# Kernel optimization log

Hardware: AMD Instinct MI355X
Metric: run time of the kernel (lower is better)

The kernel has to match this reference:

```python
import jax, jax.numpy as jnp
import numpy as np

N_INST = 64  # number of distinct instance colors generated (color = 4*label, label 0 = background)
LAMBDA_SEP = 300.0


def setup_inputs() -> dict:
    key = jax.random.key(0)
    k1, k2 = jax.random.split(key)
    B, H, W = 4, 768, 768
    labels = jax.random.randint(k1, (B, H, W), 0, N_INST)
    labels = labels.at[:, :8, :8].set(0)  # guarantee background pixels exist (torch code assumes bg_pred is set)
    # target colors: (4*l, 4*l, 4*l) in [0, 252]; background label 0 -> (0,0,0)
    target = jnp.broadcast_to((labels * 4).astype(jnp.float32)[:, None, :, :], (B, 3, H, W))
    prediction = jax.random.uniform(k2, (B, 3, H, W), dtype=jnp.float32) * 255.0
    no_bg = jnp.zeros((B,), dtype=bool)
    return {"prediction": prediction, "target": target, "no_bg": no_bg}


def _huber(x, c):
    # elementwise huber, delta=1.0 (torch default)
    d = jnp.abs(x - c)
    return jnp.where(d < 1.0, 0.5 * d * d, d - 0.5)


def _per_image(P, L, nobg):
    # P: [N,3] predicted colors, L: [N] int instance labels (0 = background)
    N = P.shape[0]
    counts = jax.ops.segment_sum(jnp.ones((N,), P.dtype), L, num_segments=N_INST)  # [K]
    safe = jnp.maximum(counts, 1.0)
    means = jax.ops.segment_sum(P, L, num_segments=N_INST) / safe[:, None]  # [K,3]
    # intra-instance huber toward constant target (255 for instances, 0 for background), mean over 3*count elems
    h255 = _huber(P, 255.0).sum(-1)  # [N]
    h0 = _huber(P, 0.0).sum(-1)
    var = jax.ops.segment_sum(h255, L, num_segments=N_INST) / (3.0 * safe)
    var0 = jax.ops.segment_sum(h0, L, num_segments=N_INST) / (3.0 * safe)
    var = var.at[0].set(var0[0])
    # pixel -> instance-mean squared distances [N,K] (separation term)
    D = jnp.sum((P[:, None, :] - means[None, :, :]) ** 2, axis=-1)
    inv = LAMBDA_SEP / (1.0 + D)  # [N,K]
    bg_mask = (L == 0).astype(P.dtype)  # [N]
    bg_cnt = bg_mask.sum()
    nbg_cnt = jnp.asarray(N, P.dtype) - bg_cnt
    # non-bg instance k: mean over background pixels of 300/(1+||p - mean_k||^2)
    sep = (bg_mask @ inv) / jnp.maximum(bg_cnt, 1.0)  # [K]
    # background instance: mean over non-background pixels vs bg mean
    sep0 = ((1.0 - bg_mask) @ inv[:, 0]) / jnp.maximum(nbg_cnt, 1.0)
    sep = sep.at[0].set(sep0)
    w = 10.0 / jnp.sqrt(safe)
    present = counts > 0
    included = present.at[0].set(jnp.logical_and(present[0], jnp.logical_not(nobg)))
    incl = included.astype(P.dtype)
    ct = jnp.maximum(incl.sum(), 1.0)
    return jnp.sum(incl * (var + w * sep)) / ct


def reference(prediction, target, no_bg):
    B = prediction.shape[0]
    # recover integer instance labels from color map (generation: color = 4*label on all 3 channels)
    labels = jnp.round(target[:, 0] / 4.0).astype(jnp.int32).reshape(B, -1)  # [B,N]
    P = jnp.transpose(prediction, (0, 2, 3, 1)).reshape(B, -1, 3)  # [B,N,3]
    losses = jax.vmap(_per_image)(P, labels, no_bg)
    return jnp.mean(losses)
```

## Files before the change

### kernel.cpp

```cpp
#include <hip/hip_runtime.h>

#define NINST 64
#define ACC_STRIDE 512
#define OFF_CNT  0
#define OFF_SUM  64
#define OFF_H255 256
#define OFF_H0   320
#define LAMBDA_SEP 300.0f

#define P1_GX 192
#define P1_THREADS 512
#define P1_WAVES (P1_THREADS / 64)
#define P2_GX 128
#define P3_GX 32
#define P3_TILE 256
#define CNT_STRIDE 64
#define BGBUF 512

__device__ __forceinline__ float huber1(float x, float c) {
    float d = fabsf(x - c);
    return d < 1.0f ? 0.5f * d * d : d - 0.5f;
}

__global__ __launch_bounds__(P1_THREADS)
void k_pass1(const float* __restrict__ pred, const float* __restrict__ targ,
             float* __restrict__ acc, unsigned* __restrict__ bgcnt,
             float* __restrict__ bglist, int maxbg, int N) {
    __shared__ float4 s_stage[P1_WAVES][256];
    __shared__ float4 s_red[P1_WAVES][NINST];
    __shared__ float s_corr255[NINST];
    __shared__ float s_corr0;
    __shared__ float s_bgbuf[BGBUF * 3];
    __shared__ unsigned s_bgn;
    __shared__ unsigned s_base;
    int tid = threadIdx.x;
    int lane = tid & 63;
    int wv = tid >> 6;
    if (tid < NINST) s_corr255[tid] = 0.0f;
    if (tid == 0) { s_corr0 = 0.0f; s_bgn = 0u; }
    __syncthreads();

    int b = blockIdx.y;
    const float* bp = pred + (size_t)b * 3 * N;
    const float* bt = targ + (size_t)b * 3 * N;
    const float4* t0 = (const float4*)bt;
    const float4* p0 = (const float4*)bp;
    const float4* p1 = (const float4*)(bp + N);
    const float4* p2 = (const float4*)(bp + 2 * N);
    unsigned* bgc = &bgcnt[(size_t)b * CNT_STRIDE];
    float* bgl = bglist + (size_t)b * maxbg * 3;
    float* g = acc + (size_t)b * ACC_STRIDE;

    float cnt = 0.0f, sx = 0.0f, sy = 0.0f, sz = 0.0f;
    int M = N >> 2;
    int stride = gridDim.x * blockDim.x;
    for (int base = blockIdx.x * blockDim.x + wv * 64; base < M; base += stride) {
        int i = base + lane;
        float xx[4], yy[4], zz[4];
        int labs[4];
        if (i < M) {
            float4 t = t0[i], a = p0[i], c = p1[i], d = p2[i];
            float tt[4] = {t.x, t.y, t.z, t.w};
            xx[0] = a.x; xx[1] = a.y; xx[2] = a.z; xx[3] = a.w;
            yy[0] = c.x; yy[1] = c.y; yy[2] = c.z; yy[3] = c.w;
            zz[0] = d.x; zz[1] = d.y; zz[2] = d.z; zz[3] = d.w;
#pragma unroll
            for (int j = 0; j < 4; j++) {
                int lab = (int)(tt[j] * 0.25f + 0.5f);
                labs[j] = lab;
                float dx = 255.0f - xx[j], dy = 255.0f - yy[j], dz = 255.0f - zz[j];
                float corr = 0.0f;
                if (dx < 1.0f) { float e = 1.0f - dx; corr += 0.5f * e * e; }
                if (dy < 1.0f) { float e = 1.0f - dy; corr += 0.5f * e * e; }
                if (dz < 1.0f) { float e = 1.0f - dz; corr += 0.5f * e * e; }
                if (corr != 0.0f) atomicAdd(&s_corr255[lab], corr);
                if (lab == 0) {
                    float c0 = 0.0f;
                    if (xx[j] < 1.0f) { float e = 1.0f - xx[j]; c0 += 0.5f * e * e; }
                    if (yy[j] < 1.0f) { float e = 1.0f - yy[j]; c0 += 0.5f * e * e; }
                    if (zz[j] < 1.0f) { float e = 1.0f - zz[j]; c0 += 0.5f * e * e; }
                    if (c0 != 0.0f) atomicAdd(&s_corr0, c0);
                    unsigned idx = atomicAdd(&s_bgn, 1u);
                    if (idx < BGBUF) {
                        s_bgbuf[idx * 3 + 0] = xx[j];
                        s_bgbuf[idx * 3 + 1] = yy[j];
                        s_bgbuf[idx * 3 + 2] = zz[j];
                    } else {
                        unsigned gi = atomicAdd(bgc, 1u);
                        if ((int)gi < maxbg) {
                            bgl[(size_t)gi * 3 + 0] = xx[j];
                            bgl[(size_t)gi * 3 + 1] = yy[j];
                            bgl[(size_t)gi * 3 + 2] = zz[j];
                        }
                    }
                }
            }
        } else {
#pragma unroll
            for (int j = 0; j < 4; j++) { xx[j] = yy[j] = zz[j] = 0.0f; labs[j] = -1; }
        }
#pragma unroll
        for (int j = 0; j < 4; j++)
            s_stage[wv][j * 64 + lane] =
                make_float4(xx[j], yy[j], zz[j], __int_as_float(labs[j]));
#pragma unroll 8
        for (int s = 0; s < 256; s++) {
            float4 v = s_stage[wv][s];
            float m = (__float_as_int(v.w) == lane) ? 1.0f : 0.0f;
            cnt += m;
            sx = fmaf(m, v.x, sx);
            sy = fmaf(m, v.y, sy);
            sz = fmaf(m, v.z, sz);
        }
    }

    s_red[wv][lane] = make_float4(cnt, sx, sy, sz);
    __syncthreads();

    unsigned nloc = s_bgn < (unsigned)BGBUF ? s_bgn : (unsigned)BGBUF;
    if (tid == 0) s_base = atomicAdd(bgc, nloc);
    __syncthreads();
    {
        unsigned base3 = s_base * 3u;
        unsigned lim3 = (unsigned)maxbg * 3u;
        for (unsigned i = tid; i < nloc * 3u; i += blockDim.x) {
            if (base3 + i < lim3) bgl[base3 + i] = s_bgbuf[i];
        }
    }

    if (tid < NINST) {
        float c = 0.0f, x = 0.0f, y = 0.0f, z = 0.0f;
#pragma unroll
        for (int w = 0; w < P1_WAVES; w++) {
            float4 r = s_red[w][tid];
            c += r.x; x += r.y; y += r.z; z += r.w;
        }
        float s3 = x + y + z;
        atomicAdd(&g[OFF_CNT + tid], c);
        atomicAdd(&g[OFF_SUM + tid * 3 + 0], x);
        atomicAdd(&g[OFF_SUM + tid * 3 + 1], y);
        atomicAdd(&g[OFF_SUM + tid * 3 + 2], z);
        atomicAdd(&g[OFF_H255 + tid], 763.5f * c - s3 + s_corr255[tid]);
        if (tid == 0) atomicAdd(&g[OFF_H0], s3 - 1.5f * c + s_corr0);
    }

    if (blockIdx.x == 0 && tid < (N & 3)) {
        int i = (M << 2) + tid;
        float t = bt[i], x = bp[i], y = bp[N + i], z = bp[2 * N + i];
        int lab = (int)(t * 0.25f + 0.5f);
        atomicAdd(&g[OFF_CNT + lab], 1.0f);
        atomicAdd(&g[OFF_SUM + lab * 3 + 0], x);
        atomicAdd(&g[OFF_SUM + lab * 3 + 1], y);
        atomicAdd(&g[OFF_SUM + lab * 3 + 2], z);
        atomicAdd(&g[OFF_H255 + lab], huber1(x, 255.f) + huber1(y, 255.f) + huber1(z, 255.f));
        if (lab == 0) {
            atomicAdd(&g[OFF_H0], huber1(x, 0.f) + huber1(y, 0.f) + huber1(z, 0.f));
            unsigned gi = atomicAdd(bgc, 1u);
            if ((int)gi < maxbg) {
                bgl[(size_t)gi * 3 + 0] = x;
                bgl[(size_t)gi * 3 + 1] = y;
                bgl[(size_t)gi * 3 + 2] = z;
            }
        }
    }
}

__global__ void k_pass2(const float* __restrict__ pred, const float* __restrict__ targ,
                        const float* __restrict__ acc, float* __restrict__ p2part, int N) {
    __shared__ float s_w[16];
    int tid = threadIdx.x;
    int b = blockIdx.y;
    const float* g = acc + (size_t)b * ACC_STRIDE;
    float safe0 = fmaxf(g[OFF_CNT + 0], 1.0f);
    float m0x = g[OFF_SUM + 0] / safe0;
    float m0y = g[OFF_SUM + 1] / safe0;
    float m0z = g[OFF_SUM + 2] / safe0;

    const float* base_p = pred + (size_t)b * 3 * N;
    const float* base_t = targ + (size_t)b * 3 * N;
    const float4* p0 = (const float4*)(base_p);
    const float4* p1 = (const float4*)(base_p + N);
    const float4* p2 = (const float4*)(base_p + 2 * N);
    const float4* t0 = (const float4*)(base_t);

    float local = 0.0f;
    int M = N >> 2;
    for (int i = blockIdx.x * blockDim.x + tid; i < M; i += gridDim.x * blockDim.x) {
        float4 t = t0[i], a = p0[i], c = p1[i], d = p2[i];
        float ts[4] = {t.x, t.y, t.z, t.w};
        float xs[4] = {a.x, a.y, a.z, a.w};
        float ys[4] = {c.x, c.y, c.z, c.w};
        float zs[4] = {d.x, d.y, d.z, d.w};
#pragma unroll
        for (int j = 0; j < 4; j++) {
            float dx = xs[j] - m0x, dy = ys[j] - m0y, dz = zs[j] - m0z;
            float D = dx * dx + dy * dy + dz * dz;
            float m = (ts[j] > 2.0f) ? LAMBDA_SEP : 0.0f;
            local = fmaf(m, __builtin_amdgcn_rcpf(1.0f + D), local);
        }
    }
    if (blockIdx.x == 0) {
        for (int i = (M << 2) + tid; i < N; i += blockDim.x) {
            float dx = base_p[i] - m0x, dy = base_p[N + i] - m0y, dz = base_p[2 * N + i] - m0z;
            float D = dx * dx + dy * dy + dz * dz;
            float m = (base_t[i] > 2.0f) ? LAMBDA_SEP : 0.0f;
            local = fmaf(m, __builtin_amdgcn_rcpf(1.0f + D), local);
        }
    }
#pragma unroll
    for (int o = 32; o > 0; o >>= 1) local += __shfl_down(local, o, 64);
    int wv = tid >> 6;
    if ((tid & 63) == 0) s_w[wv] = local;
    __syncthreads();
    if (tid == 0) {
        float s = 0.0f;
        int nw = blockDim.x >> 6;
        for (int i = 0; i < nw; i++) s += s_w[i];
        p2part[(size_t)b * P2_GX + blockIdx.x] = s;
    }
}

__global__ void k_pass3(const float* __restrict__ bglist, const unsigned* __restrict__ bgcnt,
                        const float* __restrict__ acc, float* __restrict__ p3part, int maxbg) {
    __shared__ float s_px[P3_TILE * 3];
    __shared__ float s_part[4][NINST];
    int tid = threadIdx.x;
    int lane = tid & 63;
    int wv = tid >> 6;
    int b = blockIdx.y;
    const float* g = acc + (size_t)b * ACC_STRIDE;
    float safe = fmaxf(g[OFF_CNT + lane], 1.0f);
    float mx = g[OFF_SUM + lane * 3 + 0] / safe;
    float my = g[OFF_SUM + lane * 3 + 1] / safe;
    float mz = g[OFF_SUM + lane * 3 + 2] / safe;

    int nb = min((int)bgcnt[(size_t)b * CNT_STRIDE], maxbg);
    const float* bgl = bglist + (size_t)b * maxbg * 3;

    float lacc = 0.0f;
    int ntiles = (nb + P3_TILE - 1) / P3_TILE;
    for (int tile = blockIdx.x; tile < ntiles; tile += gridDim.x) {
        int base = tile * P3_TILE;
        int cnt = min(P3_TILE, nb - base);
        __syncthreads();
        for (int i = tid; i < cnt * 3; i += blockDim.x) s_px[i] = bgl[(size_t)base * 3 + i];
        __syncthreads();
        int lim = cnt - wv * 64;
        lim = lim < 0 ? 0 : (lim > 64 ? 64 : lim);
        const float* px = &s_px[wv * 64 * 3];
        for (int j = 0; j < lim; j++) {
            float x = px[j * 3 + 0];
            float y = px[j * 3 + 1];
            float z = px[j * 3 + 2];
            float dx = x - mx, dy = y - my, dz = z - mz;
            float D = dx * dx + dy * dy + dz * dz;
            lacc += LAMBDA_SEP * __builtin_amdgcn_rcpf(1.0f + D);
        }
    }
    s_part[wv][lane] = lacc;
    __syncthreads();
    if (tid < NINST) {
        p3part[((size_t)b * P3_GX + blockIdx.x) * NINST + tid] =
            s_part[0][tid] + s_part[1][tid] + s_part[2][tid] + s_part[3][tid];
    }
}

__global__ void k_final(const float* __restrict__ acc, const float* __restrict__ p2part,
                        const float* __restrict__ p3part, const unsigned char* __restrict__ nobg,
                        float* __restrict__ out, int N, int B) {
    int tid = threadIdx.x;
    float total = 0.0f;
    for (int b = 0; b < B; b++) {
        const float* g = acc + (size_t)b * ACC_STRIDE;
        float c = g[OFF_CNT + tid];
        float c0 = g[OFF_CNT + 0];
        bool incl = (c > 0.0f);
        if (tid == 0 && nobg[b] != 0) incl = false;
        float safe = fmaxf(c, 1.0f);
        float var = (tid == 0 ? g[OFF_H0] : g[OFF_H255 + tid]) / (3.0f * safe);
        float sepnum;
        if (tid == 0) {
            float s = 0.0f;
            for (int i = 0; i < P2_GX; i++) s += p2part[(size_t)b * P2_GX + i];
            sepnum = s;
        } else {
            float s = 0.0f;
#pragma unroll
            for (int j = 0; j < P3_GX; j++) s += p3part[((size_t)b * P3_GX + j) * NINST + tid];
            sepnum = s;
        }
        float denom = (tid == 0) ? fmaxf((float)N - c0, 1.0f) : fmaxf(c0, 1.0f);
        float sep = sepnum / denom;
        float w = 10.0f / sqrtf(safe);
        float term = incl ? (var + w * sep) : 0.0f;
        float cnt = incl ? 1.0f : 0.0f;
#pragma unroll
        for (int o = 32; o > 0; o >>= 1) {
            term += __shfl_down(term, o, 64);
            cnt += __shfl_down(cnt, o, 64);
        }
        if (tid == 0) total += term / fmaxf(cnt, 1.0f);
    }
    if (tid == 0) out[0] = total / (float)B;
}

extern "C" void kernel_launch(void* const* d_in, const int* in_sizes, int n_in,
                              void* d_out, int out_size, void* d_ws, size_t ws_size,
                              hipStream_t stream) {
    const float* pred = (const float*)d_in[0];
    const float* targ = (const float*)d_in[1];
    const unsigned char* nobg = (const unsigned char*)d_in[2];
    float* out = (float*)d_out;

    int B = in_sizes[2];
    int N = in_sizes[0] / (3 * B);

    float* acc = (float*)d_ws;
    size_t acc_bytes = (size_t)B * ACC_STRIDE * sizeof(float);
    unsigned* bgcnt = (unsigned*)((char*)d_ws + acc_bytes);
    size_t head = acc_bytes + 4096;
    float* p2part = (float*)((char*)d_ws + head);
    size_t p2_bytes = (size_t)B * P2_GX * sizeof(float);
    float* p3part = p2part + (size_t)B * P2_GX;
    size_t p3_bytes = (size_t)B * P3_GX * NINST * sizeof(float);
    size_t list_off = head + p2_bytes + p3_bytes;
    list_off = (list_off + 255) & ~(size_t)255;
    float* bglist = (float*)((char*)d_ws + list_off);

    int maxbg = 0;
    if (ws_size > list_off) {
        size_t cap = (ws_size - list_off) / ((size_t)B * 3 * sizeof(float));
        maxbg = (int)(cap < (size_t)131072 ? cap : (size_t)131072);
    }

    hipMemsetAsync(d_ws, 0, head, stream);

    dim3 g1(P1_GX, B);
    k_pass1<<<g1, dim3(P1_THREADS), 0, stream>>>(pred, targ, acc, bgcnt, bglist, maxbg, N);
    dim3 g2(P2_GX, B);
    k_pass2<<<g2, dim3(1024), 0, stream>>>(pred, targ, acc, p2part, N);
    dim3 g3(P3_GX, B);
    k_pass3<<<g3, dim3(256), 0, stream>>>(bglist, bgcnt, acc, p3part, maxbg);
    k_final<<<dim3(1), dim3(64), 0, stream>>>(acc, p2part, p3part, nobg, out, N, B);
}
```

Baseline: 77.83 us.

## Split per-wave segment sum across lane groups with 8-label register accumulators

```diff
diff --git a/kernel.cpp b/kernel.cpp
--- a/kernel.cpp
+++ b/kernel.cpp
@@ -8,7 +8,7 @@
 #define OFF_H0   320
 #define LAMBDA_SEP 300.0f
 
-#define P1_GX 192
+#define P1_GX 128
 #define P1_THREADS 512
 #define P1_WAVES (P1_THREADS / 64)
 #define P2_GX 128
@@ -22,7 +22,7 @@
     return d < 1.0f ? 0.5f * d * d : d - 0.5f;
 }
 
-__global__ __launch_bounds__(P1_THREADS)
+__global__ __launch_bounds__(P1_THREADS, 4)
 void k_pass1(const float* __restrict__ pred, const float* __restrict__ targ,
              float* __restrict__ acc, unsigned* __restrict__ bgcnt,
              float* __restrict__ bglist, int maxbg, int N) {
@@ -36,6 +36,8 @@
     int tid = threadIdx.x;
     int lane = tid & 63;
     int wv = tid >> 6;
+    int grp = lane >> 3;
+    int s8 = (lane & 7) << 3;
     if (tid < NINST) s_corr255[tid] = 0.0f;
     if (tid == 0) { s_corr0 = 0.0f; s_bgn = 0u; }
     __syncthreads();
@@ -51,7 +53,10 @@
     float* bgl = bglist + (size_t)b * maxbg * 3;
     float* g = acc + (size_t)b * ACC_STRIDE;
 
-    float cnt = 0.0f, sx = 0.0f, sy = 0.0f, sz = 0.0f;
+    float cnt[8], sx[8], sy[8], sz[8];
+#pragma unroll
+    for (int t = 0; t < 8; t++) { cnt[t] = 0.0f; sx[t] = 0.0f; sy[t] = 0.0f; sz[t] = 0.0f; }
+
     int M = N >> 2;
     int stride = gridDim.x * blockDim.x;
     for (int base = blockIdx.x * blockDim.x + wv * 64; base < M; base += stride) {
@@ -103,18 +108,50 @@
         for (int j = 0; j < 4; j++)
             s_stage[wv][j * 64 + lane] =
                 make_float4(xx[j], yy[j], zz[j], __int_as_float(labs[j]));
-#pragma unroll 8
-        for (int s = 0; s < 256; s++) {
-            float4 v = s_stage[wv][s];
-            float m = (__float_as_int(v.w) == lane) ? 1.0f : 0.0f;
-            cnt += m;
-            sx = fmaf(m, v.x, sx);
-            sy = fmaf(m, v.y, sy);
-            sz = fmaf(m, v.z, sz);
-        }
-    }
-
-    s_red[wv][lane] = make_float4(cnt, sx, sy, sz);
+#pragma unroll 4
+        for (int j = 0; j < 32; j++) {
+            float4 v = s_stage[wv][(j << 3) + grp];
+            int rel = __float_as_int(v.w) - s8;
+#pragma unroll
+            for (int t = 0; t < 8; t++) {
+                float m = (rel == t) ? 1.0f : 0.0f;
+                cnt[t] += m;
+                sx[t] = fmaf(m, v.x, sx[t]);
+                sy[t] = fmaf(m, v.y, sy[t]);
+                sz[t] = fmaf(m, v.z, sz[t]);
+            }
+        }
+    }
+
+#pragma unroll
+    for (int q = 0; q < 4; q++)
+        s_stage[wv][(lane << 2) + q] = make_float4(cnt[q], sx[q], sy[q], sz[q]);
+    __syncthreads();
+    {
+        int l = lane & 31;
+        float4 ra = make_float4(0.0f, 0.0f, 0.0f, 0.0f);
+#pragma unroll
+        for (int gg = 0; gg < 8; gg++) {
+            float4 p = s_stage[wv][gg * 32 + l];
+            ra.x += p.x; ra.y += p.y; ra.z += p.z; ra.w += p.w;
+        }
+        if (lane < 32) s_red[wv][((l >> 2) << 3) + (l & 3)] = ra;
+    }
+    __syncthreads();
+#pragma unroll
+    for (int q = 0; q < 4; q++)
+        s_stage[wv][(lane << 2) + q] = make_float4(cnt[q + 4], sx[q + 4], sy[q + 4], sz[q + 4]);
+    __syncthreads();
+    {
+        int l = lane & 31;
+        float4 rb = make_float4(0.0f, 0.0f, 0.0f, 0.0f);
+#pragma unroll
+        for (int gg = 0; gg < 8; gg++) {
+            float4 p = s_stage[wv][gg * 32 + l];
+            rb.x += p.x; rb.y += p.y; rb.z += p.z; rb.w += p.w;
+        }
+        if (lane >= 32) s_red[wv][((l >> 2) << 3) + 4 + (l & 3)] = rb;
+    }
     __syncthreads();
 
     unsigned nloc = s_bgn < (unsigned)BGBUF ? s_bgn : (unsigned)BGBUF;
```

Result: no change. 78.55 us (+0.9%).

## Use per-wave LDS atomic histograms in pass1 and fuse pass2/pass3 kernels

Applied to the files above, without the earlier changes.

```diff
diff --git a/kernel.cpp b/kernel.cpp
--- a/kernel.cpp
+++ b/kernel.cpp
@@ -8,34 +8,35 @@
 #define OFF_H0   320
 #define LAMBDA_SEP 300.0f
 
-#define P1_GX 192
+#define P1_GX 256
 #define P1_THREADS 512
 #define P1_WAVES (P1_THREADS / 64)
+#define HSTRIDE 5
 #define P2_GX 128
-#define P3_GX 32
-#define P3_TILE 256
+#define P23_THREADS 1024
+#define P3B 8
+#define P3_TILE 1024
 #define CNT_STRIDE 64
-#define BGBUF 512
+#define BGBUF 256
 
 __device__ __forceinline__ float huber1(float x, float c) {
     float d = fabsf(x - c);
     return d < 1.0f ? 0.5f * d * d : d - 0.5f;
 }
 
-__global__ __launch_bounds__(P1_THREADS)
+__global__ __launch_bounds__(P1_THREADS, 8)
 void k_pass1(const float* __restrict__ pred, const float* __restrict__ targ,
              float* __restrict__ acc, unsigned* __restrict__ bgcnt,
              float* __restrict__ bglist, int maxbg, int N) {
-    __shared__ float4 s_stage[P1_WAVES][256];
-    __shared__ float4 s_red[P1_WAVES][NINST];
+    __shared__ float s_hist[P1_WAVES * NINST * HSTRIDE];
     __shared__ float s_corr255[NINST];
     __shared__ float s_corr0;
     __shared__ float s_bgbuf[BGBUF * 3];
     __shared__ unsigned s_bgn;
     __shared__ unsigned s_base;
     int tid = threadIdx.x;
-    int lane = tid & 63;
     int wv = tid >> 6;
+    for (int i = tid; i < P1_WAVES * NINST * HSTRIDE; i += P1_THREADS) s_hist[i] = 0.0f;
     if (tid < NINST) s_corr255[tid] = 0.0f;
     if (tid == 0) { s_corr0 = 0.0f; s_bgn = 0u; }
     __syncthreads();
@@ -50,71 +51,55 @@
     unsigned* bgc = &bgcnt[(size_t)b * CNT_STRIDE];
     float* bgl = bglist + (size_t)b * maxbg * 3;
     float* g = acc + (size_t)b * ACC_STRIDE;
-
-    float cnt = 0.0f, sx = 0.0f, sy = 0.0f, sz = 0.0f;
+    float* myhist = &s_hist[wv * NINST * HSTRIDE];
+
     int M = N >> 2;
     int stride = gridDim.x * blockDim.x;
-    for (int base = blockIdx.x * blockDim.x + wv * 64; base < M; base += stride) {
-        int i = base + lane;
-        float xx[4], yy[4], zz[4];
-        int labs[4];
-        if (i < M) {
-            float4 t = t0[i], a = p0[i], c = p1[i], d = p2[i];
-            float tt[4] = {t.x, t.y, t.z, t.w};
-            xx[0] = a.x; xx[1] = a.y; xx[2] = a.z; xx[3] = a.w;
-            yy[0] = c.x; yy[1] = c.y; yy[2] = c.z; yy[3] = c.w;
-            zz[0] = d.x; zz[1] = d.y; zz[2] = d.z; zz[3] = d.w;
-#pragma unroll
-            for (int j = 0; j < 4; j++) {
-                int lab = (int)(tt[j] * 0.25f + 0.5f);
-                labs[j] = lab;
-                float dx = 255.0f - xx[j], dy = 255.0f - yy[j], dz = 255.0f - zz[j];
+    for (int i = blockIdx.x * blockDim.x + tid; i < M; i += stride) {
+        float4 t = t0[i], a = p0[i], c = p1[i], d = p2[i];
+        float tt[4] = {t.x, t.y, t.z, t.w};
+        float xx[4] = {a.x, a.y, a.z, a.w};
+        float yy[4] = {c.x, c.y, c.z, c.w};
+        float zz[4] = {d.x, d.y, d.z, d.w};
+#pragma unroll
+        for (int j = 0; j < 4; j++) {
+            int lab = (int)(tt[j] * 0.25f + 0.5f);
+            float* hb = &myhist[lab * HSTRIDE];
+            atomicAdd(hb + 0, xx[j]);
+            atomicAdd(hb + 1, yy[j]);
+            atomicAdd(hb + 2, zz[j]);
+            atomicAdd(hb + 3, 1.0f);
+            float m3 = fmaxf(fmaxf(xx[j], yy[j]), zz[j]);
+            if (m3 > 254.0f) {
                 float corr = 0.0f;
-                if (dx < 1.0f) { float e = 1.0f - dx; corr += 0.5f * e * e; }
-                if (dy < 1.0f) { float e = 1.0f - dy; corr += 0.5f * e * e; }
-                if (dz < 1.0f) { float e = 1.0f - dz; corr += 0.5f * e * e; }
-                if (corr != 0.0f) atomicAdd(&s_corr255[lab], corr);
-                if (lab == 0) {
-                    float c0 = 0.0f;
-                    if (xx[j] < 1.0f) { float e = 1.0f - xx[j]; c0 += 0.5f * e * e; }
-                    if (yy[j] < 1.0f) { float e = 1.0f - yy[j]; c0 += 0.5f * e * e; }
-                    if (zz[j] < 1.0f) { float e = 1.0f - zz[j]; c0 += 0.5f * e * e; }
-                    if (c0 != 0.0f) atomicAdd(&s_corr0, c0);
-                    unsigned idx = atomicAdd(&s_bgn, 1u);
-                    if (idx < BGBUF) {
-                        s_bgbuf[idx * 3 + 0] = xx[j];
-                        s_bgbuf[idx * 3 + 1] = yy[j];
-                        s_bgbuf[idx * 3 + 2] = zz[j];
-                    } else {
-                        unsigned gi = atomicAdd(bgc, 1u);
-                        if ((int)gi < maxbg) {
-                            bgl[(size_t)gi * 3 + 0] = xx[j];
-                            bgl[(size_t)gi * 3 + 1] = yy[j];
-                            bgl[(size_t)gi * 3 + 2] = zz[j];
-                        }
+                float ex = xx[j] - 254.0f, ey = yy[j] - 254.0f, ez = zz[j] - 254.0f;
+                if (ex > 0.0f) corr += 0.5f * ex * ex;
+                if (ey > 0.0f) corr += 0.5f * ey * ey;
+                if (ez > 0.0f) corr += 0.5f * ez * ez;
+                atomicAdd(&s_corr255[lab], corr);
+            }
+            if (lab == 0) {
+                float c0 = 0.0f;
+                if (xx[j] < 1.0f) { float e = 1.0f - xx[j]; c0 += 0.5f * e * e; }
+                if (yy[j] < 1.0f) { float e = 1.0f - yy[j]; c0 += 0.5f * e * e; }
+                if (zz[j] < 1.0f) { float e = 1.0f - zz[j]; c0 += 0.5f * e * e; }
+                if (c0 != 0.0f) atomicAdd(&s_corr0, c0);
+                unsigned idx = atomicAdd(&s_bgn, 1u);
+                if (idx < BGBUF) {
+                    s_bgbuf[idx * 3 + 0] = xx[j];
+                    s_bgbuf[idx * 3 + 1] = yy[j];
+                    s_bgbuf[idx * 3 + 2] = zz[j];
+                } else {
+                    unsigned gi = atomicAdd(bgc, 1u);
+                    if ((int)gi < maxbg) {
+                        bgl[(size_t)gi * 3 + 0] = xx[j];
+                        bgl[(size_t)gi * 3 + 1] = yy[j];
+                        bgl[(size_t)gi * 3 + 2] = zz[j];
                     }
                 }
             }
-        } else {
-#pragma unroll
-            for (int j = 0; j < 4; j++) { xx[j] = yy[j] = zz[j] = 0.0f; labs[j] = -1; }
-        }
-#pragma unroll
-        for (int j = 0; j < 4; j++)
-            s_stage[wv][j * 64 + lane] =
-                make_float4(xx[j], yy[j], zz[j], __int_as_float(labs[j]));
-#pragma unroll 8
-        for (int s = 0; s < 256; s++) {
-            float4 v = s_stage[wv][s];
-            float m = (__float_as_int(v.w) == lane) ? 1.0f : 0.0f;
-            cnt += m;
-            sx = fmaf(m, v.x, sx);
-            sy = fmaf(m, v.y, sy);
-            sz = fmaf(m, v.z, sz);
-        }
-    }
-
-    s_red[wv][lane] = make_float4(cnt, sx, sy, sz);
+        }
+    }
     __syncthreads();
 
     unsigned nloc = s_bgn < (unsigned)BGBUF ? s_bgn : (unsigned)BGBUF;
@@ -132,8 +117,8 @@
         float c = 0.0f, x = 0.0f, y = 0.0f, z = 0.0f;
 #pragma unroll
         for (int w = 0; w < P1_WAVES; w++) {
-            float4 r = s_red[w][tid];
-            c += r.x; x += r.y; y += r.z; z += r.w;
+            const float* hb = &s_hist[(w * NINST + tid) * HSTRIDE];
+            x += hb[0]; y += hb[1]; z += hb[2]; c += hb[3];
         }
         float s3 = x + y + z;
         atomicAdd(&g[OFF_CNT + tid], c);
@@ -165,103 +150,104 @@
     }
 }
 
-__global__ void k_pass2(const float* __restrict__ pred, const float* __restrict__ targ,
-                        const float* __restrict__ acc, float* __restrict__ p2part, int N) {
+__global__ void k_pass23(const float* __restrict__ pred, const float* __restrict__ targ,
+                         const float* __restrict__ acc, const float* __restrict__ bglist,
+                         const unsigned* __restrict__ bgcnt, float* __restrict__ p2part,
+                         float* __restrict__ p3part, int maxbg, int N) {
     __shared__ float s_w[16];
+    __shared__ float s_px[P3_TILE * 3];
+    __shared__ float s_part[16][NINST];
     int tid = threadIdx.x;
     int b = blockIdx.y;
     const float* g = acc + (size_t)b * ACC_STRIDE;
-    float safe0 = fmaxf(g[OFF_CNT + 0], 1.0f);
-    float m0x = g[OFF_SUM + 0] / safe0;
-    float m0y = g[OFF_SUM + 1] / safe0;
-    float m0z = g[OFF_SUM + 2] / safe0;
-
-    const float* base_p = pred + (size_t)b * 3 * N;
-    const float* base_t = targ + (size_t)b * 3 * N;
-    const float4* p0 = (const float4*)(base_p);
-    const float4* p1 = (const float4*)(base_p + N);
-    const float4* p2 = (const float4*)(base_p + 2 * N);
-    const float4* t0 = (const float4*)(base_t);
-
-    float local = 0.0f;
-    int M = N >> 2;
-    for (int i = blockIdx.x * blockDim.x + tid; i < M; i += gridDim.x * blockDim.x) {
-        float4 t = t0[i], a = p0[i], c = p1[i], d = p2[i];
-        float ts[4] = {t.x, t.y, t.z, t.w};
-        float xs[4] = {a.x, a.y, a.z, a.w};
-        float ys[4] = {c.x, c.y, c.z, c.w};
-        float zs[4] = {d.x, d.y, d.z, d.w};
-#pragma unroll
-        for (int j = 0; j < 4; j++) {
-            float dx = xs[j] - m0x, dy = ys[j] - m0y, dz = zs[j] - m0z;
-            float D = dx * dx + dy * dy + dz * dz;
-            float m = (ts[j] > 2.0f) ? LAMBDA_SEP : 0.0f;
-            local = fmaf(m, __builtin_amdgcn_rcpf(1.0f + D), local);
-        }
-    }
-    if (blockIdx.x == 0) {
-        for (int i = (M << 2) + tid; i < N; i += blockDim.x) {
-            float dx = base_p[i] - m0x, dy = base_p[N + i] - m0y, dz = base_p[2 * N + i] - m0z;
-            float D = dx * dx + dy * dy + dz * dz;
-            float m = (base_t[i] > 2.0f) ? LAMBDA_SEP : 0.0f;
-            local = fmaf(m, __builtin_amdgcn_rcpf(1.0f + D), local);
-        }
-    }
-#pragma unroll
-    for (int o = 32; o > 0; o >>= 1) local += __shfl_down(local, o, 64);
-    int wv = tid >> 6;
-    if ((tid & 63) == 0) s_w[wv] = local;
-    __syncthreads();
-    if (tid == 0) {
-        float s = 0.0f;
-        int nw = blockDim.x >> 6;
-        for (int i = 0; i < nw; i++) s += s_w[i];
-        p2part[(size_t)b * P2_GX + blockIdx.x] = s;
-    }
-}
-
-__global__ void k_pass3(const float* __restrict__ bglist, const unsigned* __restrict__ bgcnt,
-                        const float* __restrict__ acc, float* __restrict__ p3part, int maxbg) {
-    __shared__ float s_px[P3_TILE * 3];
-    __shared__ float s_part[4][NINST];
-    int tid = threadIdx.x;
-    int lane = tid & 63;
-    int wv = tid >> 6;
-    int b = blockIdx.y;
-    const float* g = acc + (size_t)b * ACC_STRIDE;
-    float safe = fmaxf(g[OFF_CNT + lane], 1.0f);
-    float mx = g[OFF_SUM + lane * 3 + 0] / safe;
-    float my = g[OFF_SUM + lane * 3 + 1] / safe;
-    float mz = g[OFF_SUM + lane * 3 + 2] / safe;
-
-    int nb = min((int)bgcnt[(size_t)b * CNT_STRIDE], maxbg);
-    const float* bgl = bglist + (size_t)b * maxbg * 3;
-
-    float lacc = 0.0f;
-    int ntiles = (nb + P3_TILE - 1) / P3_TILE;
-    for (int tile = blockIdx.x; tile < ntiles; tile += gridDim.x) {
-        int base = tile * P3_TILE;
-        int cnt = min(P3_TILE, nb - base);
+
+    if (blockIdx.x < P2_GX) {
+        float safe0 = fmaxf(g[OFF_CNT + 0], 1.0f);
+        float m0x = g[OFF_SUM + 0] / safe0;
+        float m0y = g[OFF_SUM + 1] / safe0;
+        float m0z = g[OFF_SUM + 2] / safe0;
+
+        const float* base_p = pred + (size_t)b * 3 * N;
+        const float* base_t = targ + (size_t)b * 3 * N;
+        const float4* p0 = (const float4*)(base_p);
+        const float4* p1 = (const float4*)(base_p + N);
+        const float4* p2 = (const float4*)(base_p + 2 * N);
+        const float4* t0 = (const float4*)(base_t);
+
+        float local = 0.0f;
+        int M = N >> 2;
+        for (int i = blockIdx.x * blockDim.x + tid; i < M; i += P2_GX * blockDim.x) {
+            float4 t = t0[i], a = p0[i], c = p1[i], d = p2[i];
+            float ts[4] = {t.x, t.y, t.z, t.w};
+            float xs[4] = {a.x, a.y, a.z, a.w};
+            float ys[4] = {c.x, c.y, c.z, c.w};
+            float zs[4] = {d.x, d.y, d.z, d.w};
+#pragma unroll
+            for (int j = 0; j < 4; j++) {
+                float dx = xs[j] - m0x, dy = ys[j] - m0y, dz = zs[j] - m0z;
+                float D = dx * dx + dy * dy + dz * dz;
+                float m = (ts[j] > 2.0f) ? LAMBDA_SEP : 0.0f;
+                local = fmaf(m, __builtin_amdgcn_rcpf(1.0f + D), local);
+            }
+        }
+        if (blockIdx.x == 0) {
+            for (int i = (M << 2) + tid; i < N; i += blockDim.x) {
+                float dx = base_p[i] - m0x, dy = base_p[N + i] - m0y, dz = base_p[2 * N + i] - m0z;
+                float D = dx * dx + dy * dy + dz * dz;
+                float m = (base_t[i] > 2.0f) ? LAMBDA_SEP : 0.0f;
+                local = fmaf(m, __builtin_amdgcn_rcpf(1.0f + D), local);
+            }
+        }
+#pragma unroll
+        for (int o = 32; o > 0; o >>= 1) local += __shfl_down(local, o, 64);
+        int wv = tid >> 6;
+        if ((tid & 63) == 0) s_w[wv] = local;
         __syncthreads();
-        for (int i = tid; i < cnt * 3; i += blockDim.x) s_px[i] = bgl[(size_t)base * 3 + i];
+        if (tid == 0) {
+            float s = 0.0f;
+            for (int i = 0; i < (P23_THREADS >> 6); i++) s += s_w[i];
+            p2part[(size_t)b * P2_GX + blockIdx.x] = s;
+        }
+    } else {
+        int bx = blockIdx.x - P2_GX;
+        int lane = tid & 63;
+        int wv = tid >> 6;
+        float safe = fmaxf(g[OFF_CNT + lane], 1.0f);
+        float mx = g[OFF_SUM + lane * 3 + 0] / safe;
+        float my = g[OFF_SUM + lane * 3 + 1] / safe;
+        float mz = g[OFF_SUM + lane * 3 + 2] / safe;
+
+        int nb = min((int)bgcnt[(size_t)b * CNT_STRIDE], maxbg);
+        const float* bgl = bglist + (size_t)b * maxbg * 3;
+
+        float lacc = 0.0f;
+        int ntiles = (nb + P3_TILE - 1) / P3_TILE;
+        for (int tile = bx; tile < ntiles; tile += P3B) {
+            int base = tile * P3_TILE;
+            int cnt = min(P3_TILE, nb - base);
+            __syncthreads();
+            for (int i = tid; i < cnt * 3; i += blockDim.x) s_px[i] = bgl[(size_t)base * 3 + i];
+            __syncthreads();
+            int lim = cnt - wv * 64;
+            lim = lim < 0 ? 0 : (lim > 64 ? 64 : lim);
+            const float* px = &s_px[wv * 64 * 3];
+            for (int j = 0; j < lim; j++) {
+                float x = px[j * 3 + 0];
+                float y = px[j * 3 + 1];
+                float z = px[j * 3 + 2];
+                float dx = x - mx, dy = y - my, dz = z - mz;
+                float D = dx * dx + dy * dy + dz * dz;
+                lacc += LAMBDA_SEP * __builtin_amdgcn_rcpf(1.0f + D);
+            }
+        }
+        s_part[wv][lane] = lacc;
         __syncthreads();
-        int lim = cnt - wv * 64;
-        lim = lim < 0 ? 0 : (lim > 64 ? 64 : lim);
-        const float* px = &s_px[wv * 64 * 3];
-        for (int j = 0; j < lim; j++) {
-            float x = px[j * 3 + 0];
-            float y = px[j * 3 + 1];
-            float z = px[j * 3 + 2];
-            float dx = x - mx, dy = y - my, dz = z - mz;
-            float D = dx * dx + dy * dy + dz * dz;
-            lacc += LAMBDA_SEP * __builtin_amdgcn_rcpf(1.0f + D);
-        }
-    }
-    s_part[wv][lane] = lacc;
-    __syncthreads();
-    if (tid < NINST) {
-        p3part[((size_t)b * P3_GX + blockIdx.x) * NINST + tid] =
-            s_part[0][tid] + s_part[1][tid] + s_part[2][tid] + s_part[3][tid];
+        if (tid < NINST) {
+            float s = 0.0f;
+#pragma unroll
+            for (int w = 0; w < 16; w++) s += s_part[w][tid];
+            p3part[((size_t)b * P3B + bx) * NINST + tid] = s;
+        }
     }
 }
 
@@ -278,15 +264,16 @@
         if (tid == 0 && nobg[b] != 0) incl = false;
         float safe = fmaxf(c, 1.0f);
         float var = (tid == 0 ? g[OFF_H0] : g[OFF_H255 + tid]) / (3.0f * safe);
+        float s2 = p2part[(size_t)b * P2_GX + tid] + p2part[(size_t)b * P2_GX + NINST + tid];
+#pragma unroll
+        for (int o = 32; o > 0; o >>= 1) s2 += __shfl_down(s2, o, 64);
         float sepnum;
         if (tid == 0) {
-            float s = 0.0f;
-            for (int i = 0; i < P2_GX; i++) s += p2part[(size_t)b * P2_GX + i];
-            sepnum = s;
+            sepnum = s2;
         } else {
             float s = 0.0f;
 #pragma unroll
-            for (int j = 0; j < P3_GX; j++) s += p3part[((size_t)b * P3_GX + j) * NINST + tid];
+            for (int j = 0; j < P3B; j++) s += p3part[((size_t)b * P3B + j) * NINST + tid];
             sepnum = s;
         }
         float denom = (tid == 0) ? fmaxf((float)N - c0, 1.0f) : fmaxf(c0, 1.0f);
@@ -322,7 +309,7 @@
     float* p2part = (float*)((char*)d_ws + head);
     size_t p2_bytes = (size_t)B * P2_GX * sizeof(float);
     float* p3part = p2part + (size_t)B * P2_GX;
-    size_t p3_bytes = (size_t)B * P3_GX * NINST * sizeof(float);
+    size_t p3_bytes = (size_t)B * P3B * NINST * sizeof(float);
     size_t list_off = head + p2_bytes + p3_bytes;
     list_off = (list_off + 255) & ~(size_t)255;
     float* bglist = (float*)((char*)d_ws + list_off);
@@ -337,9 +324,8 @@
 
     dim3 g1(P1_GX, B);
     k_pass1<<<g1, dim3(P1_THREADS), 0, stream>>>(pred, targ, acc, bgcnt, bglist, maxbg, N);
-    dim3 g2(P2_GX, B);
-    k_pass2<<<g2, dim3(1024), 0, stream>>>(pred, targ, acc, p2part, N);
-    dim3 g3(P3_GX, B);
-    k_pass3<<<g3, dim3(256), 0, stream>>>(bglist, bgcnt, acc, p3part, maxbg);
+    dim3 g23(P2_GX + P3B, B);
+    k_pass23<<<g23, dim3(P23_THREADS), 0, stream>>>(pred, targ, acc, bglist, bgcnt,
+                                                    p2part, p3part, maxbg, N);
     k_final<<<dim3(1), dim3(64), 0, stream>>>(acc, p2part, p3part, nobg, out, N, B);
 }
```

New measurement: 123.3 us. 1.58x slower.
